# Optimization experiments

Measured on AMD Instinct MI355X. Metric: run time of the kernel, lower is better.

## Reference

```python
import jax, jax.numpy as jnp
import numpy as np


def setup_inputs() -> dict:
    key = jax.random.key(0)
    k1, k2, k3 = jax.random.split(key, 3)
    B, T = 4, 4096
    n_blocks, bs, rem = 1024, 4, 3
    n = n_blocks * bs + rem  # 4099 = min(n, m); full last-dim size
    x = jax.random.normal(k1, (B, T, n), dtype=jnp.float32)
    # matches torch init: 0.1 * randn
    blocks = 0.1 * jax.random.normal(k2, (n_blocks, bs, bs), dtype=jnp.float32)
    diag_remainder = 0.1 * jax.random.normal(k3, (rem,), dtype=jnp.float32)
    return {"x": x, "blocks": blocks, "diag_remainder": diag_remainder, "n": n}


def reference(x, blocks, diag_remainder, n):
    # BlockCore.apply_to_vector: y = D @ x where D is block-diagonal
    # (dense block_size x block_size blocks) plus a diagonal remainder.
    n_blocks, bs, _ = blocks.shape
    block_region_end = n_blocks * bs
    r = diag_remainder.shape[0]
    batch_shape = x.shape[:-1]

    # block region: [..., n_blocks, bs]; y_j = sum_k blocks[b][j,k] * x_k
    xb = x[..., :block_region_end].reshape(*batch_shape, n_blocks, bs)
    y_blocks = jnp.einsum('...nk,njk->...nj', xb, blocks)
    y_blocks = y_blocks.reshape(*batch_shape, block_region_end)

    # remainder diagonal: elementwise multiply
    y_rem = x[..., block_region_end:block_region_end + r] * diag_remainder

    y = jnp.concatenate([y_blocks, y_rem], axis=-1)
    if y.shape[-1] < n:  # zero-pad up to n (static shapes)
        pad = jnp.zeros((*batch_shape, n - y.shape[-1]), dtype=x.dtype)
        y = jnp.concatenate([y, pad], axis=-1)
    return y
```

## Files before the change

### kernel.cpp

```cpp
#include <hip/hip_runtime.h>

constexpr int N_BLOCKS = 1024;
constexpr int BS       = 4;
constexpr int REM      = 3;
constexpr int ROW      = N_BLOCKS * BS + REM;
constexpr int GROUPS   = N_BLOCKS + 1;
constexpr unsigned ROWS  = 4u * 4096u;
constexpr unsigned TOTAL = ROWS * GROUPS;

__global__ __launch_bounds__(256) void blockcore_kernel(
    const float* __restrict__ x,
    const float* __restrict__ blocks,
    const float* __restrict__ diag,
    float* __restrict__ y)
{
    unsigned w = blockIdx.x * 256u + threadIdx.x;
    if (w >= TOTAL) return;

    unsigned row = w / GROUPS;
    unsigned g   = w - row * GROUPS;

    const float* xr = x + (size_t)row * ROW;
    float*       yr = y + (size_t)row * ROW;

    if (g < N_BLOCKS) {
        const int base = g * BS;
        const float x0 = xr[base + 0];
        const float x1 = xr[base + 1];
        const float x2 = xr[base + 2];
        const float x3 = xr[base + 3];

        const float4* bp = reinterpret_cast<const float4*>(blocks + (size_t)g * 16);
        const float4 r0 = bp[0];
        const float4 r1 = bp[1];
        const float4 r2 = bp[2];
        const float4 r3 = bp[3];

        yr[base + 0] = r0.x * x0 + r0.y * x1 + r0.z * x2 + r0.w * x3;
        yr[base + 1] = r1.x * x0 + r1.y * x1 + r1.z * x2 + r1.w * x3;
        yr[base + 2] = r2.x * x0 + r2.y * x1 + r2.z * x2 + r2.w * x3;
        yr[base + 3] = r3.x * x0 + r3.y * x1 + r3.z * x2 + r3.w * x3;
    } else {
        const int base = N_BLOCKS * BS;
        yr[base + 0] = xr[base + 0] * diag[0];
        yr[base + 1] = xr[base + 1] * diag[1];
        yr[base + 2] = xr[base + 2] * diag[2];
    }
}

extern "C" void kernel_launch(void* const* d_in, const int* in_sizes, int n_in,
                              void* d_out, int out_size, void* d_ws, size_t ws_size,
                              hipStream_t stream) {
    const float* x      = (const float*)d_in[0];
    const float* blocks = (const float*)d_in[1];
    const float* diag   = (const float*)d_in[2];
    float*       y      = (float*)d_out;

    const unsigned nblk = (TOTAL + 255u) / 256u;
    blockcore_kernel<<<dim3(nblk), dim3(256), 0, stream>>>(x, blocks, diag, y);
}
```

Baseline: 463.6 us.

## Tile block-diagonal apply over row chunks with per-thread output and register-resident block rows

Replaces the one-thread-per-group kernel with a tiled kernel in which each block handles 64 groups across 128 rows. Each thread owns one output element, keeps its block row in registers, and loops over the rows, so block loads and per-element index division disappear. The remainder diagonal moves into a separate small kernel. In exchange there is an extra launch, and each x element is now read by four threads, which relies on the cache to absorb the duplicate loads.

```diff
diff --git a/kernel.cpp b/kernel.cpp
--- a/kernel.cpp
+++ b/kernel.cpp
@@ -1,51 +1,52 @@
 #include <hip/hip_runtime.h>
 
-constexpr int N_BLOCKS = 1024;
-constexpr int BS       = 4;
-constexpr int REM      = 3;
-constexpr int ROW      = N_BLOCKS * BS + REM;
-constexpr int GROUPS   = N_BLOCKS + 1;
-constexpr unsigned ROWS  = 4u * 4096u;
-constexpr unsigned TOTAL = ROWS * GROUPS;
+constexpr int ROW      = 4099;
+constexpr int ROWS     = 16384;
+constexpr int GCH      = 64;
+constexpr int NGCH     = 1024 / GCH;
+constexpr int RCH      = 128;
+constexpr int NRCH     = ROWS / RCH;
 
-__global__ __launch_bounds__(256) void blockcore_kernel(
+__global__ __launch_bounds__(256) void blockcore_main(
     const float* __restrict__ x,
     const float* __restrict__ blocks,
+    float* __restrict__ y)
+{
+    const int gchunk = blockIdx.x & (NGCH - 1);
+    const int rchunk = blockIdx.x >> 4;
+    const int t = threadIdx.x;
+    const int q = t >> 2;
+    const int j = t & 3;
+    const int g = gchunk * GCH + q;
+
+    const float4 b = *reinterpret_cast<const float4*>(blocks + (size_t)g * 16 + (size_t)j * 4);
+
+    const float* xp = x + (size_t)rchunk * RCH * ROW + (size_t)4 * g;
+    float*       yp = y + (size_t)rchunk * RCH * ROW + (size_t)4 * g + j;
+
+    #pragma unroll 4
+    for (int r = 0; r < RCH; ++r) {
+        const float x0 = xp[0];
+        const float x1 = xp[1];
+        const float x2 = xp[2];
+        const float x3 = xp[3];
+        *yp = b.x * x0 + b.y * x1 + b.z * x2 + b.w * x3;
+        xp += ROW;
+        yp += ROW;
+    }
+}
+
+__global__ __launch_bounds__(256) void blockcore_rem(
+    const float* __restrict__ x,
     const float* __restrict__ diag,
     float* __restrict__ y)
 {
-    unsigned w = blockIdx.x * 256u + threadIdx.x;
-    if (w >= TOTAL) return;
-
-    unsigned row = w / GROUPS;
-    unsigned g   = w - row * GROUPS;
-
-    const float* xr = x + (size_t)row * ROW;
-    float*       yr = y + (size_t)row * ROW;
-
-    if (g < N_BLOCKS) {
-        const int base = g * BS;
-        const float x0 = xr[base + 0];
-        const float x1 = xr[base + 1];
-        const float x2 = xr[base + 2];
-        const float x3 = xr[base + 3];
-
-        const float4* bp = reinterpret_cast<const float4*>(blocks + (size_t)g * 16);
-        const float4 r0 = bp[0];
-        const float4 r1 = bp[1];
-        const float4 r2 = bp[2];
-        const float4 r3 = bp[3];
-
-        yr[base + 0] = r0.x * x0 + r0.y * x1 + r0.z * x2 + r0.w * x3;
-        yr[base + 1] = r1.x * x0 + r1.y * x1 + r1.z * x2 + r1.w * x3;
-        yr[base + 2] = r2.x * x0 + r2.y * x1 + r2.z * x2 + r2.w * x3;
-        yr[base + 3] = r3.x * x0 + r3.y * x1 + r3.z * x2 + r3.w * x3;
-    } else {
-        const int base = N_BLOCKS * BS;
-        yr[base + 0] = xr[base + 0] * diag[0];
-        yr[base + 1] = xr[base + 1] * diag[1];
-        yr[base + 2] = xr[base + 2] * diag[2];
-    }
+    const int idx = blockIdx.x * 256 + threadIdx.x;
+    if (idx >= ROWS * 3) return;
+    const int r = idx / 3;
+    const int i = idx - r * 3;
+    const size_t off = (size_t)r * ROW + 4096 + i;
+    y[off] = x[off] * diag[i];
 }
 
 extern "C" void kernel_launch(void* const* d_in, const int* in_sizes, int n_in,
@@ -56,6 +57,6 @@
     const float* diag   = (const float*)d_in[2];
     float*       y      = (float*)d_out;
 
-    const unsigned nblk = (TOTAL + 255u) / 256u;
-    blockcore_kernel<<<dim3(nblk), dim3(256), 0, stream>>>(x, blocks, diag, y);
+    blockcore_main<<<dim3(NGCH * NRCH), dim3(256), 0, stream>>>(x, blocks, y);
+    blockcore_rem<<<dim3((ROWS * 3 + 255) / 256), dim3(256), 0, stream>>>(x, diag, y);
 }
```

After: 466.0 us. About the same (+0.5%).
